# Kernel tuning notes

Hardware: AMD Instinct MI355X
Metric: run time of the kernel (lower is better)

## Reference

```python
import jax, jax.numpy as jnp
import numpy as np

DIM = 1024
NUM_HEAD = 8
INNER = DIM // NUM_HEAD
B, L = 2, 2048
EPS = 1e-5  # GroupNorm default eps


def _xavier(key, out_d, in_d, gain=0.01):
    std = gain * np.sqrt(2.0 / (in_d + out_d))
    return (jax.random.normal(key, (out_d, in_d), jnp.float32) * std)


def setup_inputs() -> dict:
    key = jax.random.key(0)
    ks = jax.random.split(key, 12)
    x = jax.random.normal(ks[0], (B, L, DIM), jnp.float32)
    hidden = jax.random.normal(ks[1], (B, NUM_HEAD, INNER), jnp.float32)
    # dt bias: inv-softplus of dt ~ LogUniform(0.001, 0.1), as in __init__
    dt = jnp.exp(jax.random.uniform(ks[2], (NUM_HEAD,), jnp.float32,
                                    minval=np.log(0.001), maxval=np.log(0.1)))
    b_dt = dt + jnp.log1p(-jnp.exp(-dt))
    ln_a = jnp.log(jax.random.uniform(ks[3], (NUM_HEAD,), jnp.float32, minval=1.0, maxval=16.0))
    return {
        "x": x, "hidden": hidden,
        "W_z": _xavier(ks[4], DIM, DIM), "b_z": jnp.zeros((DIM,), jnp.float32),
        "W_z_act": _xavier(ks[5], DIM, DIM), "b_z_act": jnp.zeros((DIM,), jnp.float32),
        "W_y": _xavier(ks[6], DIM, DIM), "b_y": jnp.zeros((DIM,), jnp.float32),
        "W_y_act": _xavier(ks[7], DIM, DIM), "b_y_act": jnp.zeros((DIM,), jnp.float32),
        "W_dt": _xavier(ks[8], NUM_HEAD, DIM), "b_dt": b_dt,
        "ln_a": ln_a,
        "gn_w": jnp.ones((NUM_HEAD,), jnp.float32), "gn_b": jnp.zeros((NUM_HEAD,), jnp.float32),
    }


def reference(x, hidden, W_z, b_z, W_z_act, b_z_act, W_y, b_y, W_y_act, b_y_act,
              W_dt, b_dt, ln_a, gn_w, gn_b):
    b, l, d = x.shape
    nh, inner = NUM_HEAD, d // NUM_HEAD
    silu = jax.nn.silu
    xf = x.astype(jnp.float32)
    # gated input projection -> z: [b,l,h,i]
    z = ((xf @ W_z.T + b_z) * silu(xf @ W_z_act.T + b_z_act)).reshape(b, l, nh, inner)
    # log-decay per step: [b,l,h]
    ln_da = -jnp.exp(ln_a) * jax.nn.softplus(xf @ W_dt.T + b_dt)
    # einops.repeat 'b l h -> b l m h' then torch .tril(-1) (masks over LAST TWO dims (m,h))
    ln_da_masked = jnp.tril(jnp.broadcast_to(ln_da[:, :, None, :], (b, l, l, nh)), k=-1)
    # rfft/irfft conv with ones == prefix sum along l (dim 1)
    ln_da_masked_conv = jnp.cumsum(ln_da_masked, axis=1)
    da_masked_conv = jnp.tril(jnp.exp(ln_da_masked_conv))  # tril over (m,h), k=0
    h_inner = jnp.einsum('blmh,bmhi->blhi', da_masked_conv, z)
    # cross-chunk: cumulative decay applied to carried hidden state
    da_cum = jnp.exp(jnp.cumsum(ln_da, axis=1))  # [b,l,h]
    h_cross = jnp.einsum('blh,bhi->blhi', da_cum, hidden)
    h = h_inner + h_cross  # [b,l,h,i]
    hidden_next = h[:, -1]
    # GroupNorm(num_head groups, num_head channels) on [b*l, h, i]:
    # one channel per group -> normalize over inner dim per (token, head)
    mean = h.mean(axis=-1, keepdims=True)
    var = h.var(axis=-1, keepdims=True)
    h_norm = (h - mean) / jnp.sqrt(var + EPS) * gn_w[None, None, :, None] + gn_b[None, None, :, None]
    h_norm = h_norm.reshape(b, l, d)
    y = (h_norm @ W_y.T + b_y) * silu(xf @ W_y_act.T + b_y_act)
    return y.astype(x.dtype), hidden_next
```

## Files before the change

### kernel.cpp

```cpp
#include <hip/hip_runtime.h>
#include <stdint.h>

#define DIM   1024
#define L_SEQ 2048
#define BATCH 2
#define NH    8
#define M_TOT 4096
#define EPS_F 1e-5f

typedef __bf16 bf16x8 __attribute__((ext_vector_type(8)));
typedef unsigned short u16x8 __attribute__((ext_vector_type(8)));
typedef float f32x4 __attribute__((ext_vector_type(4)));

__device__ __forceinline__ unsigned short f2bf(float f) {
  unsigned int u = __float_as_uint(f);
  u += 0x7FFFu + ((u >> 16) & 1u);
  return (unsigned short)(u >> 16);
}

__device__ __forceinline__ f32x4 mfma_bf16(u16x8 a, u16x8 b, f32x4 c) {
  return __builtin_amdgcn_mfma_f32_16x16x32_bf16(
      __builtin_bit_cast(bf16x8, a), __builtin_bit_cast(bf16x8, b), c, 0, 0, 0);
}

__device__ __forceinline__ float silu_f(float v) {
  return v / (1.f + __expf(-v));
}

__device__ __forceinline__ void gload16(const unsigned short* g, unsigned short* l) {
  __builtin_amdgcn_global_load_lds(
      (const __attribute__((address_space(1))) unsigned int*)g,
      (__attribute__((address_space(3))) unsigned int*)l, 16, 0, 0);
}

__global__ __launch_bounds__(256) void prep_kernel(const float* __restrict__ x,
                                                   const float* __restrict__ W_dt,
                                                   const float* __restrict__ b_dt,
                                                   const float* __restrict__ ln_a,
                                                   const float4* __restrict__ wz,
                                                   const float4* __restrict__ wza,
                                                   const float4* __restrict__ wya,
                                                   float* __restrict__ ln_da,
                                                   unsigned short* __restrict__ xb,
                                                   ushort4* __restrict__ wzb,
                                                   ushort4* __restrict__ wzab,
                                                   ushort4* __restrict__ wyab,
                                                   float* __restrict__ Zs) {
  const int blk = blockIdx.x;
  const int tid = threadIdx.x;
  if (blk >= 4096) {
    const int wb = blk - 4096;
    if (wb < 2) ((f32x4*)Zs)[wb * 256 + tid] = f32x4{0.f, 0.f, 0.f, 0.f};
    int i = wb * 256 + tid;
    const float4* s; ushort4* d; int j;
    if (i < 262144)      { s = wz;  d = wzb;  j = i; }
    else if (i < 524288) { s = wza; d = wzab; j = i - 262144; }
    else                 { s = wya; d = wyab; j = i - 524288; }
    float4 f = s[j];
    d[j] = make_ushort4(f2bf(f.x), f2bf(f.y), f2bf(f.z), f2bf(f.w));
    return;
  }
  __shared__ float xs[DIM];
  const int row = blk;
  float4 f = ((const float4*)(x + (size_t)row * DIM))[tid];
  ((float4*)xs)[tid] = f;
  ((ushort4*)(xb + (size_t)row * DIM))[tid] =
      make_ushort4(f2bf(f.x), f2bf(f.y), f2bf(f.z), f2bf(f.w));
  __syncthreads();
  const int wave = tid >> 6, lane = tid & 63;
  for (int h = wave; h < NH; h += 4) {
    const float* w = W_dt + (size_t)h * DIM;
    float s = 0.f;
    for (int k = lane; k < DIM; k += 64) s += xs[k] * w[k];
    for (int off = 32; off > 0; off >>= 1) s += __shfl_down(s, off);
    if (lane == 0) {
      float t = s + b_dt[h];
      float sp = (t > 20.f) ? t : log1pf(expf(t));
      int b = row >> 11, l = row & (L_SEQ - 1);
      ln_da[(size_t)(b * NH + h) * L_SEQ + l] = -expf(ln_a[h]) * sp;
    }
  }
}

__global__ __launch_bounds__(256, 3) void gemm_all(const unsigned short* __restrict__ xb,
                                                   const unsigned short* __restrict__ Wz,
                                                   const unsigned short* __restrict__ Wza,
                                                   const unsigned short* __restrict__ Wya,
                                                   const float* __restrict__ b_z,
                                                   const float* __restrict__ b_za,
                                                   const float* __restrict__ b_ya,
                                                   float* __restrict__ Zs,
                                                   float* __restrict__ wdiag,
                                                   float* __restrict__ Sy) {
  __shared__ __align__(16) unsigned short As[128 * 64];
  __shared__ __align__(16) unsigned short Bs[128 * 64];
  __shared__ float colsum[64];

  const int tid = threadIdx.x;
  const int lane = tid & 63, wave = tid >> 6;
  const int wm = wave >> 1, wn = wave & 1;
  const int l16 = lane & 15, quad = lane >> 4;
  const int nt = blockIdx.x, mt = blockIdx.y;
  const bool isZ = (nt < 16);
  const int n0 = isZ ? nt * 64 : (nt - 16) * 128;
  const int m0 = mt * 128;

  f32x4 acc[4][4];
  const f32x4 zero = {0.f, 0.f, 0.f, 0.f};
  for (int i = 0; i < 4; ++i)
    for (int j = 0; j < 4; ++j) acc[i][j] = zero;

  for (int kt = 0; kt < 16; ++kt) {
    const int k0 = kt * 64;
    __syncthreads();
#pragma unroll
    for (int i = 0; i < 4; ++i) {
      const int s = i * 256 + tid;
      const int row = s >> 3;
      const int kc = (s & 7) ^ (row & 7);
      const size_t gcol = (size_t)(k0 + (kc << 3));
      gload16(xb + (size_t)(m0 + row) * DIM + gcol, As + ((size_t)s << 3));
      const unsigned short* bsrc;
      if (isZ) bsrc = (row < 64) ? (Wz + (size_t)(n0 + row) * DIM)
                                 : (Wza + (size_t)(n0 + row - 64) * DIM);
      else     bsrc = Wya + (size_t)(n0 + row) * DIM;
      gload16(bsrc + gcol, Bs + ((size_t)s << 3));
    }
    __syncthreads();
#pragma unroll
    for (int kk = 0; kk < 2; ++kk) {
      const int kc = kk * 4 + quad;
      u16x8 aF[4], bF[4];
#pragma unroll
      for (int rb = 0; rb < 4; ++rb) {
        const int r = wm * 64 + rb * 16 + l16;
        aF[rb] = *(const u16x8*)&As[r * 64 + ((kc ^ (r & 7)) << 3)];
      }
#pragma unroll
      for (int cb = 0; cb < 4; ++cb) {
        int r;
        if (isZ) r = (cb < 2) ? (wn * 32 + cb * 16 + l16)
                              : (64 + wn * 32 + (cb - 2) * 16 + l16);
        else     r = wn * 64 + cb * 16 + l16;
        bF[cb] = *(const u16x8*)&Bs[r * 64 + ((kc ^ (r & 7)) << 3)];
      }
#pragma unroll
      for (int rb = 0; rb < 4; ++rb)
#pragma unroll
        for (int cb = 0; cb < 4; ++cb)
          acc[rb][cb] = mfma_bf16(aF[rb], bF[cb], acc[rb][cb]);
    }
  }

  if (isZ) {
    __syncthreads();
    if (tid < 64) colsum[tid] = 0.f;
    __syncthreads();
    const int b = m0 >> 11;
#pragma unroll
    for (int cb = 0; cb < 2; ++cb) {
      const int nl = wn * 32 + cb * 16 + l16;
      const int n = n0 + nl;
      const int h = n >> 7;
      const float bz = b_z[n], ba = b_za[n];
      float ssum = 0.f;
#pragma unroll
      for (int rb = 0; rb < 4; ++rb) {
        const int mlb = wm * 64 + rb * 16 + quad * 4;
#pragma unroll
        for (int r = 0; r < 4; ++r) {
          const int l = (m0 + mlb + r) & (L_SEQ - 1);
          float u  = acc[rb][cb][r] + bz;
          float vv = acc[rb][cb + 2][r] + ba;
          if (l > h) ssum += u * silu_f(vv);
          else if (l == h)
            wdiag[(size_t)(b * NH + h) * 128 + (n & 127)] = u * silu_f(vv);
        }
      }
      atomicAdd(&colsum[nl], ssum);
    }
    __syncthreads();
    if (tid < 64) atomicAdd(&Zs[(size_t)b * DIM + n0 + tid], colsum[tid]);
  } else {
#pragma unroll
    for (int cb = 0; cb < 4; ++cb) {
      const int nl = wn * 64 + cb * 16 + l16;
      const float bb = b_ya[n0 + nl];
#pragma unroll
      for (int rb = 0; rb < 4; ++rb) {
        const int mlb = wm * 64 + rb * 16 + quad * 4;
#pragma unroll
        for (int r = 0; r < 4; ++r)
          Sy[(size_t)(m0 + mlb + r) * DIM + n0 + nl] = silu_f(acc[rb][cb][r] + bb);
      }
    }
  }
}

__global__ __launch_bounds__(64) void stats_scan(const float* __restrict__ Zs,
                                                 const float* __restrict__ hidden,
                                                 const float* __restrict__ wdiag,
                                                 const float* __restrict__ gn_w,
                                                 const float* __restrict__ ln_da,
                                                 float* __restrict__ vtg,
                                                 float* __restrict__ wtg,
                                                 float* __restrict__ alpha2,
                                                 float* __restrict__ hidden_next) {
  const int bh = blockIdx.x, b = bh >> 3, h = bh & 7;
  const int lane = threadIdx.x;
  const size_t base = (size_t)bh * 128;
  const float v0 = Zs[(size_t)b * DIM + h * 128 + lane]      + hidden[base + lane];
  const float v1 = Zs[(size_t)b * DIM + h * 128 + 64 + lane] + hidden[base + 64 + lane];
  const float w0 = wdiag[base + lane];
  const float w1 = wdiag[base + 64 + lane];

  float sv = v0 + v1, sw = w0 + w1;
  for (int off = 32; off > 0; off >>= 1) {
    sv += __shfl_down(sv, off);
    sw += __shfl_down(sw, off);
  }
  const float muv = __shfl(sv, 0) * (1.f / 128.f);
  const float muw = __shfl(sw, 0) * (1.f / 128.f);

  const float a0 = v0 - muv, a1 = v1 - muv;
  const float c0 = w0 - muw, c1 = w1 - muw;
  float rvv = a0 * a0 + a1 * a1;
  float rvw = a0 * c0 + a1 * c1;
  float rww = c0 * c0 + c1 * c1;
  for (int off = 32; off > 0; off >>= 1) {
    rvv += __shfl_down(rvv, off);
    rvw += __shfl_down(rvw, off);
    rww += __shfl_down(rww, off);
  }
  const float svv = __shfl(rvv, 0) * (1.f / 128.f);
  const float svw = __shfl(rvw, 0) * (1.f / 128.f);
  const float sww = __shfl(rww, 0) * (1.f / 128.f);

  const float gw = gn_w[h];
  vtg[base + lane] = a0 * gw;  vtg[base + 64 + lane] = a1 * gw;
  wtg[base + lane] = c0 * gw;  wtg[base + 64 + lane] = c1 * gw;

  const float* src = ln_da + (size_t)bh * L_SEQ;
  float carry = 0.f;
  for (int c = 0; c < L_SEQ / 64; ++c) {
    float val = src[c * 64 + lane];
#pragma unroll
    for (int off = 1; off < 64; off <<= 1) {
      float nv = __shfl_up(val, off);
      if (lane >= off) val += nv;
    }
    const float S = carry + val;
    const float ce = expf(S);
    const float D = rsqrtf(ce * ce * svv + 2.f * ce * svw + sww + EPS_F);
    const int l = c * 64 + lane;
    float* ap = alpha2 + ((size_t)(b * L_SEQ + l) * NH + h) * 2;
    ap[0] = ce * D;
    ap[1] = D;
    carry += __shfl(val, 63);
  }
  const float clast = expf(carry);
  hidden_next[base + lane]      = clast * v0 + w0;
  hidden_next[base + 64 + lane] = clast * v1 + w1;
}

__global__ __launch_bounds__(256) void proj_kernel(const float* __restrict__ W_y,
                                                   const float* __restrict__ vtg,
                                                   const float* __restrict__ wtg,
                                                   const float* __restrict__ gn_b,
                                                   const float* __restrict__ b_y,
                                                   float* __restrict__ Gv,
                                                   float* __restrict__ Gw,
                                                   float* __restrict__ constc) {
  const int tid = threadIdx.x, wave = tid >> 6, lane = tid & 63;
  const int n = blockIdx.x * 4 + wave;
  const float4* row = (const float4*)(W_y + (size_t)n * DIM);
  const int half = lane >> 5, l32 = lane & 31;
  float cc = 0.f;
#pragma unroll
  for (int p = 0; p < 4; ++p) {
    const int h = p * 2 + half;
    float4 wv = row[p * 64 + lane];
    const float4 va = *(const float4*)&vtg[(size_t)h * 128 + l32 * 4];
    const float4 vb = *(const float4*)&vtg[(size_t)(8 + h) * 128 + l32 * 4];
    const float4 wa = *(const float4*)&wtg[(size_t)h * 128 + l32 * 4];
    const float4 wb = *(const float4*)&wtg[(size_t)(8 + h) * 128 + l32 * 4];
    float gv0 = wv.x * va.x + wv.y * va.y + wv.z * va.z + wv.w * va.w;
    float gv1 = wv.x * vb.x + wv.y * vb.y + wv.z * vb.z + wv.w * vb.w;
    float gw0 = wv.x * wa.x + wv.y * wa.y + wv.z * wa.z + wv.w * wa.w;
    float gw1 = wv.x * wb.x + wv.y * wb.y + wv.z * wb.z + wv.w * wb.w;
    cc += (wv.x + wv.y + wv.z + wv.w) * gn_b[h];
#pragma unroll
    for (int off = 16; off > 0; off >>= 1) {
      gv0 += __shfl_down(gv0, off, 32);
      gv1 += __shfl_down(gv1, off, 32);
      gw0 += __shfl_down(gw0, off, 32);
      gw1 += __shfl_down(gw1, off, 32);
    }
    if (l32 == 0) {
      Gv[(size_t)h * DIM + n]       = gv0;
      Gv[(size_t)(8 + h) * DIM + n] = gv1;
      Gw[(size_t)h * DIM + n]       = gw0;
      Gw[(size_t)(8 + h) * DIM + n] = gw1;
    }
  }
  for (int off = 32; off > 0; off >>= 1) cc += __shfl_down(cc, off);
  if (lane == 0) constc[n] = b_y[n] + cc;
}

__global__ __launch_bounds__(256) void finalize(const float* __restrict__ alpha2,
                                                const float* __restrict__ Gv,
                                                const float* __restrict__ Gw,
                                                const float* __restrict__ constc,
                                                float* __restrict__ y) {
  const int tid = threadIdx.x;
  const int n0 = blockIdx.x * 256;
  const int m0 = blockIdx.y * 64;
  const int b = m0 >> 11;
  __shared__ float aS[64 * 16];
  ((float4*)aS)[tid] = ((const float4*)(alpha2 + (size_t)m0 * 16))[tid];
  __syncthreads();
  const int c = tid & 63;
  const int rg = tid >> 6;
  const int n = n0 + c * 4;
  f32x4 g[16 * 2];
#pragma unroll
  for (int h = 0; h < 8; ++h) {
    g[2 * h]     = *(const f32x4*)&Gv[(size_t)(b * NH + h) * DIM + n];
    g[2 * h + 1] = *(const f32x4*)&Gw[(size_t)(b * NH + h) * DIM + n];
  }
  const f32x4 cc = *(const f32x4*)&constc[n];
#pragma unroll
  for (int j = 0; j < 16; ++j) {
    const int m = m0 + rg * 16 + j;
    const float* a = &aS[(rg * 16 + j) * 16];
    f32x4 Ay = cc;
#pragma unroll
    for (int k = 0; k < 16; ++k) Ay += a[k] * g[k];
    f32x4 s = *(const f32x4*)&y[(size_t)m * DIM + n];
    *(f32x4*)&y[(size_t)m * DIM + n] = Ay * s;
  }
}

extern "C" void kernel_launch(void* const* d_in, const int* in_sizes, int n_in,
                              void* d_out, int out_size, void* d_ws, size_t ws_size,
                              hipStream_t stream) {
  const float* x      = (const float*)d_in[0];
  const float* hidden = (const float*)d_in[1];
  const float* W_z    = (const float*)d_in[2];
  const float* b_z    = (const float*)d_in[3];
  const float* W_za   = (const float*)d_in[4];
  const float* b_za   = (const float*)d_in[5];
  const float* W_y    = (const float*)d_in[6];
  const float* b_y    = (const float*)d_in[7];
  const float* W_ya   = (const float*)d_in[8];
  const float* b_ya   = (const float*)d_in[9];
  const float* W_dt   = (const float*)d_in[10];
  const float* b_dt   = (const float*)d_in[11];
  const float* ln_a   = (const float*)d_in[12];
  const float* gn_w   = (const float*)d_in[13];
  const float* gn_b   = (const float*)d_in[14];

  char* ws = (char*)d_ws;
  unsigned short* xb   = (unsigned short*)(ws);
  unsigned short* Wzb  = (unsigned short*)(ws + 8388608);
  unsigned short* Wzab = (unsigned short*)(ws + 10485760);
  unsigned short* Wyab = (unsigned short*)(ws + 12582912);
  float* ln_da  = (float*)(ws + 14680064);
  float* Zs     = (float*)(ws + 14811136);
  float* wdiag  = (float*)(ws + 14819328);
  float* vtg    = (float*)(ws + 14827520);
  float* wtg    = (float*)(ws + 14835712);
  float* Gv     = (float*)(ws + 14843904);
  float* Gw     = (float*)(ws + 14909440);
  float* constc = (float*)(ws + 14974976);
  float* alpha2 = (float*)(ws + 14979072);

  float* y = (float*)d_out;
  float* hidden_next = y + (size_t)M_TOT * DIM;

  prep_kernel<<<7168, 256, 0, stream>>>(x, W_dt, b_dt, ln_a,
                                        (const float4*)W_z, (const float4*)W_za,
                                        (const float4*)W_ya,
                                        ln_da, xb, (ushort4*)Wzb, (ushort4*)Wzab,
                                        (ushort4*)Wyab, Zs);

  gemm_all<<<dim3(24, 32), 256, 0, stream>>>(xb, Wzb, Wzab, Wyab,
                                             b_z, b_za, b_ya, Zs, wdiag, y);

  stats_scan<<<16, 64, 0, stream>>>(Zs, hidden, wdiag, gn_w, ln_da,
                                    vtg, wtg, alpha2, hidden_next);
  proj_kernel<<<256, 256, 0, stream>>>(W_y, vtg, wtg, gn_b, b_y, Gv, Gw, constc);

  finalize<<<dim3(4, 64), 256, 0, stream>>>(alpha2, Gv, Gw, constc, y);
}
```

Baseline: 179.8 us.

## Double-buffer GEMM LDS tiles with a smaller K step to overlap loads

The main GEMM loop now uses two LDS buffers with a K tile of 32 instead of one buffer with a K tile of 64. Each iteration issues the global loads for the next tile before running MFMAs on the current one, leaving one barrier per step. Source pointers and swizzled LDS read offsets are precomputed outside the loop, and the swizzle changes to a rotation suited to 4 chunks per row. The aim is to hide global-load latency behind compute. In exchange there are twice as many loop iterations, and correctness relies on the barrier waiting for the outstanding loads to finish.

```diff
diff --git a/kernel.cpp b/kernel.cpp
--- a/kernel.cpp
+++ b/kernel.cpp
@@ -92,8 +92,8 @@
                                                    float* __restrict__ Zs,
                                                    float* __restrict__ wdiag,
                                                    float* __restrict__ Sy) {
-  __shared__ __align__(16) unsigned short As[128 * 64];
-  __shared__ __align__(16) unsigned short Bs[128 * 64];
+  __shared__ __align__(16) unsigned short As[2][128 * 32];
+  __shared__ __align__(16) unsigned short Bs[2][128 * 32];
   __shared__ float colsum[64];
 
   const int tid = threadIdx.x;
@@ -105,51 +105,72 @@
   const int n0 = isZ ? nt * 64 : (nt - 16) * 128;
   const int m0 = mt * 128;
 
+  const int s0 = tid, s1 = 256 + tid;
+  const int row0 = s0 >> 2, pos0 = s0 & 3, g0 = (pos0 - (row0 >> 1)) & 3;
+  const int row1 = s1 >> 2, pos1 = s1 & 3, g1 = (pos1 - (row1 >> 1)) & 3;
+  const unsigned short* a0src = xb + (size_t)(m0 + row0) * DIM + g0 * 8;
+  const unsigned short* a1src = xb + (size_t)(m0 + row1) * DIM + g1 * 8;
+  const unsigned short* b0src;
+  const unsigned short* b1src;
+  if (isZ) {
+    b0src = (row0 < 64) ? (Wz + (size_t)(n0 + row0) * DIM) : (Wza + (size_t)(n0 + row0 - 64) * DIM);
+    b1src = (row1 < 64) ? (Wz + (size_t)(n0 + row1) * DIM) : (Wza + (size_t)(n0 + row1 - 64) * DIM);
+  } else {
+    b0src = Wya + (size_t)(n0 + row0) * DIM;
+    b1src = Wya + (size_t)(n0 + row1) * DIM;
+  }
+  b0src += g0 * 8;
+  b1src += g1 * 8;
+
+  int aOff[4], bOff[4];
+#pragma unroll
+  for (int rb = 0; rb < 4; ++rb) {
+    const int r = wm * 64 + rb * 16 + l16;
+    aOff[rb] = r * 32 + (((quad + (r >> 1)) & 3) << 3);
+  }
+#pragma unroll
+  for (int cb = 0; cb < 4; ++cb) {
+    int r;
+    if (isZ) r = (cb < 2) ? (wn * 32 + cb * 16 + l16)
+                          : (64 + wn * 32 + (cb - 2) * 16 + l16);
+    else     r = wn * 64 + cb * 16 + l16;
+    bOff[cb] = r * 32 + (((quad + (r >> 1)) & 3) << 3);
+  }
+
   f32x4 acc[4][4];
   const f32x4 zero = {0.f, 0.f, 0.f, 0.f};
   for (int i = 0; i < 4; ++i)
     for (int j = 0; j < 4; ++j) acc[i][j] = zero;
 
-  for (int kt = 0; kt < 16; ++kt) {
-    const int k0 = kt * 64;
+  gload16(a0src, &As[0][s0 << 3]);
+  gload16(b0src, &Bs[0][s0 << 3]);
+  gload16(a1src, &As[0][s1 << 3]);
+  gload16(b1src, &Bs[0][s1 << 3]);
+
+  for (int kt = 0; kt < 32; ++kt) {
+    const int cur = kt & 1;
     __syncthreads();
-#pragma unroll
-    for (int i = 0; i < 4; ++i) {
-      const int s = i * 256 + tid;
-      const int row = s >> 3;
-      const int kc = (s & 7) ^ (row & 7);
-      const size_t gcol = (size_t)(k0 + (kc << 3));
-      gload16(xb + (size_t)(m0 + row) * DIM + gcol, As + ((size_t)s << 3));
-      const unsigned short* bsrc;
-      if (isZ) bsrc = (row < 64) ? (Wz + (size_t)(n0 + row) * DIM)
-                                 : (Wza + (size_t)(n0 + row - 64) * DIM);
-      else     bsrc = Wya + (size_t)(n0 + row) * DIM;
-      gload16(bsrc + gcol, Bs + ((size_t)s << 3));
-    }
-    __syncthreads();
-#pragma unroll
-    for (int kk = 0; kk < 2; ++kk) {
-      const int kc = kk * 4 + quad;
-      u16x8 aF[4], bF[4];
-#pragma unroll
-      for (int rb = 0; rb < 4; ++rb) {
-        const int r = wm * 64 + rb * 16 + l16;
-        aF[rb] = *(const u16x8*)&As[r * 64 + ((kc ^ (r & 7)) << 3)];
-      }
-#pragma unroll
-      for (int cb = 0; cb < 4; ++cb) {
-        int r;
-        if (isZ) r = (cb < 2) ? (wn * 32 + cb * 16 + l16)
-                              : (64 + wn * 32 + (cb - 2) * 16 + l16);
-        else     r = wn * 64 + cb * 16 + l16;
-        bF[cb] = *(const u16x8*)&Bs[r * 64 + ((kc ^ (r & 7)) << 3)];
-      }
-#pragma unroll
-      for (int rb = 0; rb < 4; ++rb)
-#pragma unroll
-        for (int cb = 0; cb < 4; ++cb)
-          acc[rb][cb] = mfma_bf16(aF[rb], bF[cb], acc[rb][cb]);
-    }
+    if (kt + 1 < 32) {
+      const size_t gcol = (size_t)(kt + 1) * 32;
+      unsigned short* Ad = As[1 - cur];
+      unsigned short* Bd = Bs[1 - cur];
+      gload16(a0src + gcol, Ad + (s0 << 3));
+      gload16(b0src + gcol, Bd + (s0 << 3));
+      gload16(a1src + gcol, Ad + (s1 << 3));
+      gload16(b1src + gcol, Bd + (s1 << 3));
+    }
+    const unsigned short* Ar = As[cur];
+    const unsigned short* Br = Bs[cur];
+    u16x8 aF[4], bF[4];
+#pragma unroll
+    for (int rb = 0; rb < 4; ++rb) aF[rb] = *(const u16x8*)&Ar[aOff[rb]];
+#pragma unroll
+    for (int cb = 0; cb < 4; ++cb) bF[cb] = *(const u16x8*)&Br[bOff[cb]];
+#pragma unroll
+    for (int rb = 0; rb < 4; ++rb)
+#pragma unroll
+      for (int cb = 0; cb < 4; ++cb)
+        acc[rb][cb] = mfma_bf16(aF[rb], bF[cb], acc[rb][cb]);
   }
 
   if (isZ) {
```

Measured after the change: 183.4 us. No clear change (+2.0%).

## Parallelize stats scan across four waves and simplify GEMM tile loading

Applied to the files above, without the earlier changes.

The stats_scan kernel goes from one wave running a serial 32-chunk scan to four waves. Each wave scans 8 chunks, and a shared-memory pass computes the chunk offsets, which shortens the serial dependency chain. The GEMM tile loads now use precomputed base offsets and pointers with the same swizzle, which removes per-iteration index and branch arithmetic. Occupancy in launch bounds is raised from 3 to 4 blocks, which may tighten the register budget and cause spills.

```diff
diff --git a/kernel.cpp b/kernel.cpp
--- a/kernel.cpp
+++ b/kernel.cpp
@@ -82,7 +82,7 @@
   }
 }
 
-__global__ __launch_bounds__(256, 3) void gemm_all(const unsigned short* __restrict__ xb,
+__global__ __launch_bounds__(256, 4) void gemm_all(const unsigned short* __restrict__ xb,
                                                    const unsigned short* __restrict__ Wz,
                                                    const unsigned short* __restrict__ Wza,
                                                    const unsigned short* __restrict__ Wya,
@@ -105,27 +105,31 @@
   const int n0 = isZ ? nt * 64 : (nt - 16) * 128;
   const int m0 = mt * 128;
 
+  const int rowl = tid >> 3;
+  const int g = (tid & 7) ^ (rowl & 7);
+  const size_t aoff = (size_t)(m0 + rowl) * DIM + g * 8;
+  const size_t boff = (size_t)(n0 + rowl) * DIM + g * 8;
+  const unsigned short* bp0 = isZ ? Wz : Wya;
+  const unsigned short* bp1 = isZ ? Wza : (Wya + (size_t)64 * DIM);
+  unsigned short* AsD = As + tid * 8;
+  unsigned short* BsD = Bs + tid * 8;
+
   f32x4 acc[4][4];
   const f32x4 zero = {0.f, 0.f, 0.f, 0.f};
   for (int i = 0; i < 4; ++i)
     for (int j = 0; j < 4; ++j) acc[i][j] = zero;
 
   for (int kt = 0; kt < 16; ++kt) {
-    const int k0 = kt * 64;
+    const size_t k0 = (size_t)kt * 64;
     __syncthreads();
-#pragma unroll
-    for (int i = 0; i < 4; ++i) {
-      const int s = i * 256 + tid;
-      const int row = s >> 3;
-      const int kc = (s & 7) ^ (row & 7);
-      const size_t gcol = (size_t)(k0 + (kc << 3));
-      gload16(xb + (size_t)(m0 + row) * DIM + gcol, As + ((size_t)s << 3));
-      const unsigned short* bsrc;
-      if (isZ) bsrc = (row < 64) ? (Wz + (size_t)(n0 + row) * DIM)
-                                 : (Wza + (size_t)(n0 + row - 64) * DIM);
-      else     bsrc = Wya + (size_t)(n0 + row) * DIM;
-      gload16(bsrc + gcol, Bs + ((size_t)s << 3));
-    }
+    gload16(xb  + aoff + k0,                 AsD);
+    gload16(xb  + aoff + 32 * DIM + k0,      AsD + 2048);
+    gload16(xb  + aoff + 64 * DIM + k0,      AsD + 4096);
+    gload16(xb  + aoff + 96 * DIM + k0,      AsD + 6144);
+    gload16(bp0 + boff + k0,                 BsD);
+    gload16(bp0 + boff + 32 * DIM + k0,      BsD + 2048);
+    gload16(bp1 + boff + k0,                 BsD + 4096);
+    gload16(bp1 + boff + 32 * DIM + k0,      BsD + 6144);
     __syncthreads();
 #pragma unroll
     for (int kk = 0; kk < 2; ++kk) {
@@ -197,70 +201,100 @@
   }
 }
 
-__global__ __launch_bounds__(64) void stats_scan(const float* __restrict__ Zs,
-                                                 const float* __restrict__ hidden,
-                                                 const float* __restrict__ wdiag,
-                                                 const float* __restrict__ gn_w,
-                                                 const float* __restrict__ ln_da,
-                                                 float* __restrict__ vtg,
-                                                 float* __restrict__ wtg,
-                                                 float* __restrict__ alpha2,
-                                                 float* __restrict__ hidden_next) {
+__global__ __launch_bounds__(256) void stats_scan(const float* __restrict__ Zs,
+                                                  const float* __restrict__ hidden,
+                                                  const float* __restrict__ wdiag,
+                                                  const float* __restrict__ gn_w,
+                                                  const float* __restrict__ ln_da,
+                                                  float* __restrict__ vtg,
+                                                  float* __restrict__ wtg,
+                                                  float* __restrict__ alpha2,
+                                                  float* __restrict__ hidden_next) {
   const int bh = blockIdx.x, b = bh >> 3, h = bh & 7;
-  const int lane = threadIdx.x;
+  const int tid = threadIdx.x, wv = tid >> 6, lane = tid & 63;
+  __shared__ float csumS[32];
+  __shared__ float statS[4];
+
+  float v0 = 0.f, v1 = 0.f, w0 = 0.f, w1 = 0.f;
   const size_t base = (size_t)bh * 128;
-  const float v0 = Zs[(size_t)b * DIM + h * 128 + lane]      + hidden[base + lane];
-  const float v1 = Zs[(size_t)b * DIM + h * 128 + 64 + lane] + hidden[base + 64 + lane];
-  const float w0 = wdiag[base + lane];
-  const float w1 = wdiag[base + 64 + lane];
-
-  float sv = v0 + v1, sw = w0 + w1;
-  for (int off = 32; off > 0; off >>= 1) {
-    sv += __shfl_down(sv, off);
-    sw += __shfl_down(sw, off);
-  }
-  const float muv = __shfl(sv, 0) * (1.f / 128.f);
-  const float muw = __shfl(sw, 0) * (1.f / 128.f);
-
-  const float a0 = v0 - muv, a1 = v1 - muv;
-  const float c0 = w0 - muw, c1 = w1 - muw;
-  float rvv = a0 * a0 + a1 * a1;
-  float rvw = a0 * c0 + a1 * c1;
-  float rww = c0 * c0 + c1 * c1;
-  for (int off = 32; off > 0; off >>= 1) {
-    rvv += __shfl_down(rvv, off);
-    rvw += __shfl_down(rvw, off);
-    rww += __shfl_down(rww, off);
-  }
-  const float svv = __shfl(rvv, 0) * (1.f / 128.f);
-  const float svw = __shfl(rvw, 0) * (1.f / 128.f);
-  const float sww = __shfl(rww, 0) * (1.f / 128.f);
-
-  const float gw = gn_w[h];
-  vtg[base + lane] = a0 * gw;  vtg[base + 64 + lane] = a1 * gw;
-  wtg[base + lane] = c0 * gw;  wtg[base + 64 + lane] = c1 * gw;
+  if (wv == 0) {
+    v0 = Zs[(size_t)b * DIM + h * 128 + lane]      + hidden[base + lane];
+    v1 = Zs[(size_t)b * DIM + h * 128 + 64 + lane] + hidden[base + 64 + lane];
+    w0 = wdiag[base + lane];
+    w1 = wdiag[base + 64 + lane];
+    float sv = v0 + v1, sw = w0 + w1;
+    for (int off = 32; off > 0; off >>= 1) {
+      sv += __shfl_down(sv, off);
+      sw += __shfl_down(sw, off);
+    }
+    const float muv = __shfl(sv, 0) * (1.f / 128.f);
+    const float muw = __shfl(sw, 0) * (1.f / 128.f);
+    const float a0 = v0 - muv, a1 = v1 - muv;
+    const float c0 = w0 - muw, c1 = w1 - muw;
+    float rvv = a0 * a0 + a1 * a1;
+    float rvw = a0 * c0 + a1 * c1;
+    float rww = c0 * c0 + c1 * c1;
+    for (int off = 32; off > 0; off >>= 1) {
+      rvv += __shfl_down(rvv, off);
+      rvw += __shfl_down(rvw, off);
+      rww += __shfl_down(rww, off);
+    }
+    if (lane == 0) {
+      statS[0] = rvv * (1.f / 128.f);
+      statS[1] = rvw * (1.f / 128.f);
+      statS[2] = rww * (1.f / 128.f);
+    }
+    const float gw = gn_w[h];
+    vtg[base + lane] = a0 * gw;  vtg[base + 64 + lane] = a1 * gw;
+    wtg[base + lane] = c0 * gw;  wtg[base + 64 + lane] = c1 * gw;
+  }
 
   const float* src = ln_da + (size_t)bh * L_SEQ;
-  float carry = 0.f;
-  for (int c = 0; c < L_SEQ / 64; ++c) {
+  float vals[8];
+#pragma unroll
+  for (int j = 0; j < 8; ++j) {
+    const int c = wv * 8 + j;
     float val = src[c * 64 + lane];
 #pragma unroll
     for (int off = 1; off < 64; off <<= 1) {
       float nv = __shfl_up(val, off);
       if (lane >= off) val += nv;
     }
-    const float S = carry + val;
+    vals[j] = val;
+    if (lane == 63) csumS[c] = val;
+  }
+  __syncthreads();
+
+  if (tid < 32) {
+    float s = csumS[tid];
+    float incl = s;
+#pragma unroll
+    for (int off = 1; off < 32; off <<= 1) {
+      float nv = __shfl_up(incl, off);
+      if (tid >= off) incl += nv;
+    }
+    csumS[tid] = incl - s;
+    if (tid == 31) statS[3] = incl;
+  }
+  __syncthreads();
+
+  const float svv = statS[0], svw = statS[1], sww = statS[2];
+#pragma unroll
+  for (int j = 0; j < 8; ++j) {
+    const int c = wv * 8 + j;
+    const float S = csumS[c] + vals[j];
     const float ce = expf(S);
     const float D = rsqrtf(ce * ce * svv + 2.f * ce * svw + sww + EPS_F);
     const int l = c * 64 + lane;
     float* ap = alpha2 + ((size_t)(b * L_SEQ + l) * NH + h) * 2;
     ap[0] = ce * D;
     ap[1] = D;
-    carry += __shfl(val, 63);
-  }
-  const float clast = expf(carry);
-  hidden_next[base + lane]      = clast * v0 + w0;
-  hidden_next[base + 64 + lane] = clast * v1 + w1;
+  }
+  if (wv == 0) {
+    const float clast = expf(statS[3]);
+    hidden_next[base + lane]      = clast * v0 + w0;
+    hidden_next[base + 64 + lane] = clast * v1 + w1;
+  }
 }
 
 __global__ __launch_bounds__(256) void proj_kernel(const float* __restrict__ W_y,
@@ -387,8 +421,8 @@
   gemm_all<<<dim3(24, 32), 256, 0, stream>>>(xb, Wzb, Wzab, Wyab,
                                              b_z, b_za, b_ya, Zs, wdiag, y);
 
-  stats_scan<<<16, 64, 0, stream>>>(Zs, hidden, wdiag, gn_w, ln_da,
-                                    vtg, wtg, alpha2, hidden_next);
+  stats_scan<<<16, 256, 0, stream>>>(Zs, hidden, wdiag, gn_w, ln_da,
+                                     vtg, wtg, alpha2, hidden_next);
   proj_kernel<<<256, 256, 0, stream>>>(W_y, vtg, wtg, gn_b, b_y, Gv, Gw, constc);
 
   finalize<<<dim3(4, 64), 256, 0, stream>>>(alpha2, Gv, Gw, constc, y);
```

Result: faster. 175.0 us (-2.7%).
